# Kernel optimization log

Hardware: AMD Instinct MI355X
Metric: run time of the kernel (lower is better)

Reference implementation:

```python
import jax, jax.numpy as jnp
import numpy as np

GRID_SIZE = 300


def setup_inputs() -> dict:
    key = jax.random.key(0)
    k1, k2 = jax.random.split(key)
    N, input_dim, out_dim = 2048, 256, 256
    x = jax.random.normal(k1, (N, input_dim), dtype=jnp.float32)
    scale = 1.0 / (np.sqrt(input_dim) * np.sqrt(GRID_SIZE))
    coeffs = jax.random.normal(k2, (2, out_dim, input_dim, GRID_SIZE), dtype=jnp.float32) * scale
    bias = jnp.zeros((1, out_dim), dtype=jnp.float32)
    return {"x": x, "coeffs": coeffs, "bias": bias}


def reference(x, coeffs, bias):
    # x: [N, I]; coeffs: [2, J, I, K]; bias: [1, J]
    grid_size = coeffs.shape[-1]
    k = jnp.arange(1, grid_size + 1, dtype=x.dtype)            # [K]
    ang = x[:, :, None] * k                                    # [N, I, K]
    c = jnp.cos(ang)
    s = jnp.sin(ang)
    # einsum('dbik,djik->bj') with d=2 split into cos/sin parts
    y = jnp.einsum('bik,jik->bj', c, coeffs[0]) + jnp.einsum('bik,jik->bj', s, coeffs[1])
    y = y + bias
    return y
```

## Files before the change

kernel.cpp:

```cpp
#include <hip/hip_runtime.h>
#include <stdint.h>

#define NB 2048
#define NI 256
#define NJ 256
#define GK 300
#define KPAD 320
#define KK_PER_I (2*KPAD)
#define NKC (NI*KK_PER_I/32)
#define CH_PER_I 20
#define SPLITK 32
#define II_PER_S (NI / SPLITK)
#define BM 128

typedef __bf16 bf16x8 __attribute__((ext_vector_type(8)));
typedef __bf16 bf16x2 __attribute__((ext_vector_type(2)));
typedef float  f32x4  __attribute__((ext_vector_type(4)));

__device__ __forceinline__ void sincos2pi(float ang, float& c, float& s) {
  float r = ang * 0.15915494309189535f;
  r = r - floorf(r);
  c = __builtin_amdgcn_cosf(r);
  s = __builtin_amdgcn_sinf(r);
}

__device__ __forceinline__ unsigned int pkbf(float c, float s) {
  bf16x2 p; p.x = (__bf16)c; p.y = (__bf16)s;
  return __builtin_bit_cast(unsigned int, p);
}

__device__ __forceinline__ void rot(float& c, float& s, float cr, float sr) {
  float nc = c * cr - s * sr;
  s = s * cr + c * sr;
  c = nc;
}

__global__ __launch_bounds__(256) void convert_b(const float* __restrict__ coeffs,
                                                 unsigned int* __restrict__ bw) {
  const int bid = blockIdx.x;
  const int i  = bid >> 4;
  const int jt = bid & 15;
  const int t  = (int)threadIdx.x;
  const int n  = t & 15;
  const int gl = t >> 4;
  const int j  = jt * 16 + n;

  const float4* r0 = (const float4*)(coeffs + (size_t)(j * NI + i) * GK);
  const float4* r1 = (const float4*)(coeffs + (size_t)((NJ + j) * NI + i) * GK);

  #pragma unroll
  for (int p = 0; p < 5; p++) {
    const int g = p * 16 + gl;
    uint4 w = {0u, 0u, 0u, 0u};
    if (g < GK / 4) {
      float4 a = r0[g];
      float4 b = r1[g];
      w.x = pkbf(a.x, b.x);
      w.y = pkbf(a.y, b.y);
      w.z = pkbf(a.z, b.z);
      w.w = pkbf(a.w, b.w);
    }
    const int kc = i * 20 + (g >> 2);
    const unsigned int idx = ((unsigned int)(kc * 16 + jt) << 8) + ((g & 3) << 6) + (n << 2);
    *(uint4*)(bw + idx) = w;
  }
}

__global__ __launch_bounds__(256) void init_out(const float* __restrict__ bias,
                                                float* __restrict__ out) {
  const int tid = blockIdx.x * 256 + threadIdx.x;
  float4 b = ((const float4*)bias)[tid & 63];
  ((float4*)out)[tid] = b;
}

__global__ __launch_bounds__(256, 2) void fkan_gemm(const float* __restrict__ x,
                                                    const uint4* __restrict__ bw4,
                                                    float* __restrict__ out) {
  const int bid = blockIdx.x;
  const int mt = bid & 15;
  const int s  = bid >> 4;
  const int m0 = mt * BM;

  const int t    = (int)threadIdx.x;
  const int lane = t & 63;
  const int wave = t >> 6;
  const int wr = wave >> 1;
  const int wc = wave & 1;
  const int q  = lane >> 4;
  const int ln = lane & 15;

  f32x4 acc[4][8];
  #pragma unroll
  for (int mm = 0; mm < 4; mm++)
    #pragma unroll
    for (int nn = 0; nn < 8; nn++)
      acc[mm][nn] = (f32x4){0.f, 0.f, 0.f, 0.f};

  const uint4* bptr = bw4 + (size_t)(wc * 8) * 64 + lane;

  int kc = s * (NKC / SPLITK);
  uint4 bcur[8], bnxt[8];
  #pragma unroll
  for (int nn = 0; nn < 8; nn++) bcur[nn] = bptr[(size_t)kc * 1024 + nn * 64];

  float stc[4], sts[4], c1a[4], s1a[4], cDa[4], sDa[4];

  #pragma unroll 1
  for (int ii = 0; ii < II_PER_S; ii++) {
    const int i = s * II_PER_S + ii;
    #pragma unroll
    for (int mm = 0; mm < 4; mm++) {
      const float xv = x[(m0 + wr * 64 + mm * 16 + ln) * NI + i];
      sincos2pi(xv, c1a[mm], s1a[mm]);
      sincos2pi(13.f * xv, cDa[mm], sDa[mm]);
      sincos2pi(xv * (float)(q * 4 + 1), stc[mm], sts[mm]);
    }

    #pragma unroll 2
    for (int c = 0; c < CH_PER_I; c++) {
      const int kcn = (kc + 1 < NKC) ? kc + 1 : kc;
      #pragma unroll
      for (int nn = 0; nn < 8; nn++)
        bnxt[nn] = bptr[(size_t)kcn * 1024 + nn * 64];

      bf16x8 af[4];
      #pragma unroll
      for (int mm = 0; mm < 4; mm++) {
        float cc = stc[mm], ss = sts[mm];
        uint4 u;
        u.x = pkbf(cc, ss);
        rot(cc, ss, c1a[mm], s1a[mm]); u.y = pkbf(cc, ss);
        rot(cc, ss, c1a[mm], s1a[mm]); u.z = pkbf(cc, ss);
        rot(cc, ss, c1a[mm], s1a[mm]); u.w = pkbf(cc, ss);
        rot(cc, ss, cDa[mm], sDa[mm]); stc[mm] = cc; sts[mm] = ss;
        af[mm] = __builtin_bit_cast(bf16x8, u);
      }

      #pragma unroll
      for (int nn = 0; nn < 8; nn++) {
        const bf16x8 bfr = __builtin_bit_cast(bf16x8, bcur[nn]);
        #pragma unroll
        for (int mm = 0; mm < 4; mm++)
          acc[mm][nn] = __builtin_amdgcn_mfma_f32_16x16x32_bf16(
              af[mm], bfr, acc[mm][nn], 0, 0, 0);
      }

      #pragma unroll
      for (int nn = 0; nn < 8; nn++) bcur[nn] = bnxt[nn];
      kc++;
    }
  }

  const int r0 = m0 + wr * 64 + q * 4;
  const int c0 = wc * 128 + ln;
  #pragma unroll
  for (int mm = 0; mm < 4; mm++)
    #pragma unroll
    for (int nn = 0; nn < 8; nn++)
      #pragma unroll
      for (int r = 0; r < 4; r++)
        atomicAdd(&out[(r0 + mm * 16 + r) * NJ + c0 + nn * 16], acc[mm][nn][r]);
}

extern "C" void kernel_launch(void* const* d_in, const int* in_sizes, int n_in,
                              void* d_out, int out_size, void* d_ws, size_t ws_size,
                              hipStream_t stream) {
  const float* x      = (const float*)d_in[0];
  const float* coeffs = (const float*)d_in[1];
  const float* bias   = (const float*)d_in[2];
  float* out = (float*)d_out;
  unsigned int* bw = (unsigned int*)d_ws;

  convert_b<<<dim3(NI * 16), dim3(256), 0, stream>>>(coeffs, bw);
  init_out<<<dim3(NB * NJ / 4 / 256), dim3(256), 0, stream>>>(bias, out);
  fkan_gemm<<<dim3(16 * SPLITK), dim3(256), 0, stream>>>(x, (const uint4*)bw, out);
}
```

Before: 437.1 us.

## Remap GEMM waves to full-M column slices and transpose B conversion via LDS

The GEMM wave tiling goes from a 2x2 layout (64 rows by 128 columns per wave) to a 1x4 layout where each wave covers all 128 rows and 64 columns. Each wave now loads half as many B fragments per chunk but generates twice as many sin/cos A fragments. MFMAs are issued per A fragment so the A registers are consumed right after they are built. Separately, the coefficient conversion kernel stages packed values through a shared-memory tile so global reads are coalesced along k before writing the swizzled layout. The trade-off is less B traffic per wave in exchange for duplicated trig work for A across waves.

```diff
diff --git a/kernel.cpp b/kernel.cpp
--- a/kernel.cpp
+++ b/kernel.cpp
@@ -37,32 +37,44 @@
 
 __global__ __launch_bounds__(256) void convert_b(const float* __restrict__ coeffs,
                                                  unsigned int* __restrict__ bw) {
+  __shared__ uint4 sb[80][17];
   const int bid = blockIdx.x;
   const int i  = bid >> 4;
   const int jt = bid & 15;
   const int t  = (int)threadIdx.x;
-  const int n  = t & 15;
-  const int gl = t >> 4;
-  const int j  = jt * 16 + n;
 
-  const float4* r0 = (const float4*)(coeffs + (size_t)(j * NI + i) * GK);
-  const float4* r1 = (const float4*)(coeffs + (size_t)((NJ + j) * NI + i) * GK);
-
-  #pragma unroll
-  for (int p = 0; p < 5; p++) {
-    const int g = p * 16 + gl;
-    uint4 w = {0u, 0u, 0u, 0u};
-    if (g < GK / 4) {
-      float4 a = r0[g];
-      float4 b = r1[g];
-      w.x = pkbf(a.x, b.x);
-      w.y = pkbf(a.y, b.y);
-      w.z = pkbf(a.z, b.z);
-      w.w = pkbf(a.w, b.w);
+  {
+    const int jr = t >> 4;
+    const int gq = t & 15;
+    const int j  = jt * 16 + jr;
+    const float4* r0 = (const float4*)(coeffs + (size_t)(j * NI + i) * GK);
+    const float4* r1 = (const float4*)(coeffs + (size_t)((NJ + j) * NI + i) * GK);
+    #pragma unroll
+    for (int p = 0; p < 5; p++) {
+      const int g = p * 16 + gq;
+      uint4 w = {0u, 0u, 0u, 0u};
+      if (g < GK / 4) {
+        float4 a = r0[g];
+        float4 b = r1[g];
+        w.x = pkbf(a.x, b.x);
+        w.y = pkbf(a.y, b.y);
+        w.z = pkbf(a.z, b.z);
+        w.w = pkbf(a.w, b.w);
+      }
+      sb[g][jr] = w;
     }
-    const int kc = i * 20 + (g >> 2);
-    const unsigned int idx = ((unsigned int)(kc * 16 + jt) << 8) + ((g & 3) << 6) + (n << 2);
-    *(uint4*)(bw + idx) = w;
+  }
+  __syncthreads();
+  {
+    const int n  = t & 15;
+    const int gl = t >> 4;
+    #pragma unroll
+    for (int p = 0; p < 5; p++) {
+      const int g = p * 16 + gl;
+      const int kc = i * 20 + (g >> 2);
+      const unsigned int idx = ((unsigned int)(kc * 16 + jt) << 8) + ((g & 3) << 6) + (n << 2);
+      *(uint4*)(bw + idx) = sb[g][n];
+    }
   }
 }
 
@@ -84,33 +96,31 @@
   const int t    = (int)threadIdx.x;
   const int lane = t & 63;
   const int wave = t >> 6;
-  const int wr = wave >> 1;
-  const int wc = wave & 1;
   const int q  = lane >> 4;
   const int ln = lane & 15;
 
-  f32x4 acc[4][8];
+  f32x4 acc[8][4];
   #pragma unroll
-  for (int mm = 0; mm < 4; mm++)
+  for (int mm = 0; mm < 8; mm++)
     #pragma unroll
-    for (int nn = 0; nn < 8; nn++)
+    for (int nn = 0; nn < 4; nn++)
       acc[mm][nn] = (f32x4){0.f, 0.f, 0.f, 0.f};
 
-  const uint4* bptr = bw4 + (size_t)(wc * 8) * 64 + lane;
+  const uint4* bptr = bw4 + (size_t)(wave * 4) * 64 + lane;
 
   int kc = s * (NKC / SPLITK);
-  uint4 bcur[8], bnxt[8];
+  uint4 bcur[4], bnxt[4];
   #pragma unroll
-  for (int nn = 0; nn < 8; nn++) bcur[nn] = bptr[(size_t)kc * 1024 + nn * 64];
+  for (int nn = 0; nn < 4; nn++) bcur[nn] = bptr[(size_t)kc * 1024 + nn * 64];
 
-  float stc[4], sts[4], c1a[4], s1a[4], cDa[4], sDa[4];
+  float stc[8], sts[8], c1a[8], s1a[8], cDa[8], sDa[8];
 
   #pragma unroll 1
   for (int ii = 0; ii < II_PER_S; ii++) {
     const int i = s * II_PER_S + ii;
     #pragma unroll
-    for (int mm = 0; mm < 4; mm++) {
-      const float xv = x[(m0 + wr * 64 + mm * 16 + ln) * NI + i];
+    for (int mm = 0; mm < 8; mm++) {
+      const float xv = x[(m0 + mm * 16 + ln) * NI + i];
       sincos2pi(xv, c1a[mm], s1a[mm]);
       sincos2pi(13.f * xv, cDa[mm], sDa[mm]);
       sincos2pi(xv * (float)(q * 4 + 1), stc[mm], sts[mm]);
@@ -120,12 +130,11 @@
     for (int c = 0; c < CH_PER_I; c++) {
       const int kcn = (kc + 1 < NKC) ? kc + 1 : kc;
       #pragma unroll
-      for (int nn = 0; nn < 8; nn++)
+      for (int nn = 0; nn < 4; nn++)
         bnxt[nn] = bptr[(size_t)kcn * 1024 + nn * 64];
 
-      bf16x8 af[4];
       #pragma unroll
-      for (int mm = 0; mm < 4; mm++) {
+      for (int mm = 0; mm < 8; mm++) {
         float cc = stc[mm], ss = sts[mm];
         uint4 u;
         u.x = pkbf(cc, ss);
@@ -133,30 +142,25 @@
         rot(cc, ss, c1a[mm], s1a[mm]); u.z = pkbf(cc, ss);
         rot(cc, ss, c1a[mm], s1a[mm]); u.w = pkbf(cc, ss);
         rot(cc, ss, cDa[mm], sDa[mm]); stc[mm] = cc; sts[mm] = ss;
-        af[mm] = __builtin_bit_cast(bf16x8, u);
+        const bf16x8 af = __builtin_bit_cast(bf16x8, u);
+        #pragma unroll
+        for (int nn = 0; nn < 4; nn++)
+          acc[mm][nn] = __builtin_amdgcn_mfma_f32_16x16x32_bf16(
+              af, __builtin_bit_cast(bf16x8, bcur[nn]), acc[mm][nn], 0, 0, 0);
       }
 
       #pragma unroll
-      for (int nn = 0; nn < 8; nn++) {
-        const bf16x8 bfr = __builtin_bit_cast(bf16x8, bcur[nn]);
-        #pragma unroll
-        for (int mm = 0; mm < 4; mm++)
-          acc[mm][nn] = __builtin_amdgcn_mfma_f32_16x16x32_bf16(
-              af[mm], bfr, acc[mm][nn], 0, 0, 0);
-      }
-
-      #pragma unroll
-      for (int nn = 0; nn < 8; nn++) bcur[nn] = bnxt[nn];
+      for (int nn = 0; nn < 4; nn++) bcur[nn] = bnxt[nn];
       kc++;
     }
   }
 
-  const int r0 = m0 + wr * 64 + q * 4;
-  const int c0 = wc * 128 + ln;
+  const int r0 = m0 + q * 4;
+  const int c0 = wave * 64 + ln;
   #pragma unroll
-  for (int mm = 0; mm < 4; mm++)
+  for (int mm = 0; mm < 8; mm++)
     #pragma unroll
-    for (int nn = 0; nn < 8; nn++)
+    for (int nn = 0; nn < 4; nn++)
       #pragma unroll
       for (int r = 0; r < 4; r++)
         atomicAdd(&out[(r0 + mm * 16 + r) * NJ + c0 + nn * 16], acc[mm][nn][r]);
```

New measurement: 453.4 us. 1.04x slower.
